# Kernel optimization log

Measured on AMD Instinct MI355X. Metric: run time of the kernel, lower is better.

The kernel has to match this reference:

```python
import jax, jax.numpy as jnp
import numpy as np

N_FLUID = 16384
N_BDY = 4096
E_F = 262144
E_B = 65536
F_IN = 4
B_IN = 4
RBF_N = 8
RBF_M = 8


def _tent_basis(x, n):
    # 'linear' RBF series: tent (hat) functions on n centers spanning [-1, 1]
    c = jnp.linspace(-1.0, 1.0, n, dtype=x.dtype)
    spacing = 2.0 / (n - 1)
    return jnp.maximum(0.0, 1.0 - jnp.abs(x[:, None] - c[None, :]) / spacing)  # [E, n]


def _polar_map(d):
    # coordinateMapping='polar': (dx,dy) -> (2*r-1, theta/pi), both ~[-1,1]
    r = jnp.sqrt(jnp.sum(d * d, axis=-1) + 1e-12)
    theta = jnp.arctan2(d[:, 1], d[:, 0])
    return jnp.stack([2.0 * r - 1.0, theta / np.pi], axis=-1)


def _rbf_conv(x_src, tgt_idx, src_idx, edge_dirs, W, num_targets):
    # Continuous RBF convolution: gather source feats along edges, weight by
    # separable RBF basis of the (mapped) edge direction, scatter-sum to targets.
    # W: [n, m, c_in, c_out]; edge_dirs: [E, 2]
    n, m, cin, cout = W.shape
    mapped = _polar_map(edge_dirs)
    bu = _tent_basis(mapped[:, 0], n)                     # [E, n]
    bv = _tent_basis(mapped[:, 1], m)                     # [E, m]
    b = (bu[:, :, None] * bv[:, None, :]).reshape(edge_dirs.shape[0], n * m)  # [E, K]
    xj = x_src[src_idx]                                   # [E, c_in]
    Wk = W.reshape(n * m, cin, cout)                      # [K, c_in, c_out]

    def step(acc, kv):
        bk, wk = kv                                       # [E], [c_in, c_out]
        return acc + bk[:, None] * (xj @ wk), None

    acc0 = jnp.zeros((xj.shape[0], cout), dtype=xj.dtype)
    msgs, _ = jax.lax.scan(step, acc0, (b.T, Wk))         # [E, c_out], no [E,K,c] blowup
    return jax.ops.segment_sum(msgs, tgt_idx, num_segments=num_targets)


def _forward(fp, bp, ff, bfeat, support, W0, W1, W2, W3, W4, fc0, fc1, fc2, fc3,
             fi, fj, bf, bb):
    nf = fp.shape[0]
    # edge direction features (post radius-search math of RbfNet.forward)
    flen = jnp.clip(-(fp[fj] - fp[fi]) / support, -1.0, 1.0)   # [E_F, 2]
    blen = jnp.clip((bp[bb] - fp[bf]) / support, -1.0, 1.0)    # [E_B, 2]

    lin = jax.nn.relu(ff @ fc0)                                      # [nf, 32]
    fconv = jax.nn.relu(_rbf_conv(ff, fi, fj, flen, W0, nf))         # [nf, 32]
    bconv = jax.nn.relu(_rbf_conv(bfeat, bf, bb, blen, W1, nf))      # [nf, 32]
    ans = jnp.concatenate([lin, fconv, bconv], axis=-1)              # [nf, 96]

    # layer i=2: features 32 != 64 -> no residual, relu
    ans = jax.nn.relu(_rbf_conv(ans, fi, fj, flen, W2, nf) + ans @ fc1)
    # layer i=3: 64 == 64 -> residual, relu
    ans = jax.nn.relu(_rbf_conv(ans, fi, fj, flen, W3, nf) + ans @ fc2 + ans)
    # layer i=4 (last): no residual (64 != 2), no relu
    ans = _rbf_conv(ans, fi, fj, flen, W4, nf) + ans @ fc3
    return ans                                                        # [nf, 2]


def setup_inputs() -> dict:
    key = jax.random.key(0)
    ks = jax.random.split(key, 20)

    def xavier(k, cin, cout):
        s = float(np.sqrt(2.0 / (cin + cout)))
        return jax.random.normal(k, (cin, cout), dtype=jnp.float32) * s

    def conv_w(k, n, m, cin, cout):
        s = float(np.sqrt(2.0 / (cin + cout)) / np.sqrt(n))
        return jax.random.normal(k, (n, m, cin, cout), dtype=jnp.float32) * s

    inp = {
        'fluidPositions': jax.random.uniform(ks[0], (N_FLUID, 2), dtype=jnp.float32),
        'boundaryPositions': jax.random.uniform(ks[1], (N_BDY, 2), dtype=jnp.float32),
        'fluidFeatures': jax.random.normal(ks[2], (N_FLUID, F_IN), dtype=jnp.float32),
        'boundaryFeatures': jax.random.normal(ks[3], (N_BDY, B_IN), dtype=jnp.float32),
        'support': jnp.asarray(1.5, dtype=jnp.float32),
        'fi': jax.random.randint(ks[4], (E_F,), 0, N_FLUID, dtype=jnp.int32),
        'fj': jax.random.randint(ks[5], (E_F,), 0, N_FLUID, dtype=jnp.int32),
        'bf': jax.random.randint(ks[6], (E_B,), 0, N_FLUID, dtype=jnp.int32),
        'bb': jax.random.randint(ks[7], (E_B,), 0, N_BDY, dtype=jnp.int32),
        'W0': conv_w(ks[8], RBF_N, RBF_M, F_IN, 32),
        'W1': conv_w(ks[9], RBF_N, RBF_M, B_IN, 32),
        'W2': conv_w(ks[10], RBF_N, RBF_M, 96, 64),
        'W3': conv_w(ks[11], RBF_N, RBF_M, 64, 64),
        'W4': conv_w(ks[12], RBF_N, RBF_M, 64, 2),
        'fc0': xavier(ks[13], F_IN, 32),
        'fc1': xavier(ks[14], 96, 64),
        'fc2': xavier(ks[15], 64, 64),
        'fc3': xavier(ks[16], 64, 2),
    }
    return inp


def reference(fluidPositions, boundaryPositions, fluidFeatures, boundaryFeatures,
              support, fi, fj, bf, bb, W0, W1, W2, W3, W4, fc0, fc1, fc2, fc3):
    return _forward(fluidPositions, boundaryPositions, fluidFeatures, boundaryFeatures,
                    support, W0, W1, W2, W3, W4, fc0, fc1, fc2, fc3, fi, fj, bf, bb)
```

## Files before the change

kernel.cpp:

```cpp
#include <hip/hip_runtime.h>

#define NF 16384
#define NB 4096
#define EF 262144
#define EB 65536
#define FBLK 1024
#define BBLK 256

typedef __attribute__((ext_vector_type(8))) short bf16x8;
typedef __attribute__((ext_vector_type(4))) float f32x4;

__device__ __forceinline__ short f2b(float f) {
  unsigned u = __float_as_uint(f);
  u += 0x7fff + ((u >> 16) & 1);
  return (short)(u >> 16);
}
__device__ __forceinline__ unsigned pack2(float lo, float hi) {
  return (unsigned)(unsigned short)f2b(lo) | ((unsigned)(unsigned short)f2b(hi) << 16);
}
__device__ __forceinline__ float b2f_lo(unsigned u) {
  return __uint_as_float(u << 16);
}
__device__ __forceinline__ float b2f_hi(unsigned u) {
  return __uint_as_float(u & 0xffff0000u);
}

__global__ void __launch_bounds__(256) dual_hist(const int* __restrict__ fi,
                                                 const int* __restrict__ bfi,
                                                 int* __restrict__ fhist,
                                                 int* __restrict__ bhist) {
  int bid = blockIdx.x;
  if (bid < FBLK) {
    int e = bid * 256 + threadIdx.x;
    atomicAdd(fhist + fi[e], 1);
  } else {
    int e = (bid - FBLK) * 256 + threadIdx.x;
    atomicAdd(bhist + bfi[e], 1);
  }
}

__global__ void __launch_bounds__(1024) csr_scan2(const int* __restrict__ fhist,
                                                  const int* __restrict__ bhist,
                                                  int* __restrict__ fstart, int* __restrict__ fcur,
                                                  int* __restrict__ bstart, int* __restrict__ bcur) {
  const int* hist = blockIdx.x ? bhist : fhist;
  int* start = blockIdx.x ? bstart : fstart;
  int* cursor = blockIdx.x ? bcur : fcur;
  __shared__ int wtot[16];
  int t = threadIdx.x;
  int lane = t & 63, wv = t >> 6;
  int base = t * 16;
  int vals[16];
  int s = 0;
#pragma unroll
  for (int k = 0; k < 16; k++) { vals[k] = hist[base + k]; s += vals[k]; }
  int ss = s;
  for (int off = 1; off < 64; off <<= 1) {
    int o = __shfl_up(ss, off, 64);
    if (lane >= off) ss += o;
  }
  if (lane == 63) wtot[wv] = ss;
  __syncthreads();
  if (t < 16) {
    int v = wtot[t];
    int vv = v;
    for (int off = 1; off < 16; off <<= 1) {
      int o = __shfl_up(vv, off, 64);
      if (t >= off) vv += o;
    }
    wtot[t] = vv - v;
  }
  __syncthreads();
  int run = ss - s + wtot[wv];
#pragma unroll
  for (int k = 0; k < 16; k++) { start[base + k] = run; cursor[base + k] = run; run += vals[k]; }
  if (t == 1023) start[16384] = run;
}

__global__ void __launch_bounds__(256) dual_scatter_payload(
    const int* __restrict__ fi, const int* __restrict__ fj,
    const int* __restrict__ bfi, const int* __restrict__ bb,
    const float* __restrict__ fp, const float* __restrict__ bp,
    const float* __restrict__ supportp,
    int* __restrict__ fcur, int* __restrict__ bcur,
    unsigned* __restrict__ fpk, float4* __restrict__ fwt,
    unsigned* __restrict__ bpk, float4* __restrict__ bwt) {
  int bid = blockIdx.x;
  bool fluid = bid < FBLK;
  int e = (fluid ? bid : bid - FBLK) * 256 + threadIdx.x;
  int ti = fluid ? fi[e] : bfi[e];
  int si = fluid ? fj[e] : bb[e];
  const float2* pT2 = (const float2*)fp;
  const float2* pS2 = fluid ? (const float2*)fp : (const float2*)bp;
  float sign = fluid ? -1.f : 1.f;
  float inv_sup = 1.0f / supportp[0];
  float2 pt = pT2[ti];
  float2 ps = pS2[si];
  float dx = sign * ((ps.x - pt.x) * inv_sup);
  float dy = sign * ((ps.y - pt.y) * inv_sup);
  dx = fminf(fmaxf(dx, -1.f), 1.f);
  dy = fminf(fmaxf(dy, -1.f), 1.f);
  float r = sqrtf(dx * dx + dy * dy + 1e-12f);
  float theta;
  if (dx == 0.0f && dy == 0.0f) {
    float mag = __builtin_signbitf(dx) ? 3.14159265358979323846f : 0.0f;
    theta = __builtin_signbitf(dy) ? -mag : mag;
  } else {
    theta = atan2f(dy, dx);
  }
  float u = 2.f * r - 1.f;
  float v = theta * (1.f / 3.14159265358979323846f);
  float tu = (u + 1.f) * 3.5f;
  float tv = (v + 1.f) * 3.5f;
  int iu = min(max((int)floorf(tu), 0), 6);
  int iv = min(max((int)floorf(tv), 0), 6);
  float wu0 = fmaxf(0.f, 1.f - fabsf(tu - (float)iu));
  float wu1 = fmaxf(0.f, 1.f - fabsf(tu - (float)(iu + 1)));
  float wv0 = fmaxf(0.f, 1.f - fabsf(tv - (float)iv));
  float wv1 = fmaxf(0.f, 1.f - fabsf(tv - (float)(iv + 1)));
  unsigned pk = (unsigned)si | ((unsigned)(iu * 8 + iv) << 14);
  float4 w4 = make_float4(wu0 * wv0, wu0 * wv1, wu1 * wv0, wu1 * wv1);
  if (fluid) {
    int p = atomicAdd(fcur + ti, 1);
    fpk[p] = pk; fwt[p] = w4;
  } else {
    int p = atomicAdd(bcur + ti, 1);
    bpk[p] = pk; bwt[p] = w4;
  }
}

__global__ void __launch_bounds__(256) build_weights(
    const float* __restrict__ W2, const float* __restrict__ W3,
    const float* __restrict__ W4, const float* __restrict__ W0,
    const float* __restrict__ W1,
    short* __restrict__ BT2, short* __restrict__ BT3, short* __restrict__ BT4,
    float* __restrict__ W0T, float* __restrict__ W1T) {
  int bid = blockIdx.x;
  if (bid < 1536) {
    int tid = bid * 256 + threadIdx.x;
    int k = tid % 96, n = tid / 96;
    BT2[tid] = f2b(W2[((size_t)(n >> 6) * 96 + k) * 64 + (n & 63)]);
  } else if (bid < 2560) {
    int tid = (bid - 1536) * 256 + threadIdx.x;
    int k = tid & 63, n = tid >> 6;
    BT3[tid] = f2b(W3[((size_t)(n >> 6) * 64 + k) * 64 + (n & 63)]);
  } else if (bid < 2592) {
    int tid = (bid - 2560) * 256 + threadIdx.x;
    int k = tid & 63, n = tid >> 6;
    BT4[tid] = f2b(W4[((size_t)(n >> 1) * 64 + k) * 2 + (n & 1)]);
  } else {
    int tid = (bid - 2592) * 256 + threadIdx.x;
    int cell = tid >> 7, r = tid & 127;
    int p = r >> 3, k = (r >> 1) & 3, c = r & 1;
    int dst = cell * 128 + p * 8 + k * 2 + c;
    int src = cell * 128 + k * 32 + 2 * p + c;
    W0T[dst] = W0[src];
    W1T[dst] = W1[src];
  }
}

template <int K>
__global__ void __launch_bounds__(256, 2) gemm_bf16(
    const short* __restrict__ A, const short* __restrict__ BT,
    short* __restrict__ C, int N) {
  constexpr int KP = K + 8;
  __shared__ __align__(16) short Al[128 * KP];
  __shared__ __align__(16) short Bl[128 * KP];
  int tid = threadIdx.x;
  int lane = tid & 63;
  int w = tid >> 6;
  int m0b = blockIdx.x * 128;
  int n0b = blockIdx.y * 128;
  constexpr int ROWV = K / 8;
  for (int f = tid; f < 128 * ROWV; f += 256) {
    int r = f / ROWV, c = f % ROWV;
    *(float4*)(Al + r * KP + c * 8) = *(const float4*)(A + (size_t)(m0b + r) * K + c * 8);
    *(float4*)(Bl + r * KP + c * 8) = *(const float4*)(BT + (size_t)(n0b + r) * K + c * 8);
  }
  __syncthreads();
  int m0 = (w & 1) * 64;
  int n0 = (w >> 1) * 64;
  int fr = lane & 15;
  int kg = lane >> 4;
  f32x4 acc[4][4] = {};
#pragma unroll
  for (int kc = 0; kc < K; kc += 32) {
    bf16x8 a[4], b[4];
#pragma unroll
    for (int i = 0; i < 4; i++) {
      a[i] = *(const bf16x8*)(Al + (m0 + i * 16 + fr) * KP + kc + kg * 8);
      b[i] = *(const bf16x8*)(Bl + (n0 + i * 16 + fr) * KP + kc + kg * 8);
    }
#pragma unroll
    for (int i = 0; i < 4; i++)
#pragma unroll
      for (int j = 0; j < 4; j++)
        acc[i][j] = __builtin_amdgcn_mfma_f32_16x16x32_bf16(a[i], b[j], acc[i][j], 0, 0, 0);
  }
#pragma unroll
  for (int i = 0; i < 4; i++) {
    int row = m0b + m0 + i * 16 + (lane >> 4) * 4;
#pragma unroll
    for (int j = 0; j < 4; j++) {
      int col = n0b + n0 + j * 16 + (lane & 15);
#pragma unroll
      for (int r = 0; r < 4; r++)
        C[(size_t)(row + r) * N + col] = f2b(acc[i][j][r]);
    }
  }
}

__global__ void __launch_bounds__(256, 8) b1_stage1(
    const float* __restrict__ ff, const float* __restrict__ bfe,
    const float* __restrict__ fc0,
    const float* __restrict__ W0T, const float* __restrict__ W1T,
    const int* __restrict__ ftstart, const unsigned* __restrict__ fpk,
    const float4* __restrict__ fwt,
    const int* __restrict__ btstart, const unsigned* __restrict__ bpk,
    const float4* __restrict__ bwt,
    float* __restrict__ ans0, short* __restrict__ Xh96) {
  int lane = threadIdx.x & 63;
  int t = __builtin_amdgcn_readfirstlane(blockIdx.x * 4 + (threadIdx.x >> 6));
  int q = lane >> 4;
  int p = lane & 15;
  int cofs = (q & 1) + (q >> 1) * 8;

  auto run_side = [&](const int* st, const unsigned* pkA, const float4* wtA,
                      const float* xA, const float* WT) -> float2 {
    float2 acc = make_float2(0.f, 0.f);
    int s = __builtin_amdgcn_readfirstlane(st[t]);
    int e1 = __builtin_amdgcn_readfirstlane(st[t + 1]);
    for (int base = s; base < e1; base += 64) {
      int Ln = min(64, e1 - base);
      unsigned mypk = 0;
      float4 myw = make_float4(0.f, 0.f, 0.f, 0.f);
      float4 myx = make_float4(0.f, 0.f, 0.f, 0.f);
      if (lane < Ln) {
        mypk = pkA[base + lane];
        myw = wtA[base + lane];
        myx = *(const float4*)(xA + (size_t)(mypk & 16383) * 4);
      }
      int j = 0;
      for (; j + 3 < Ln; j += 4) {
        unsigned pk_[4];
        float wq_[4], xx_[4], xy_[4], xz_[4], xw_[4];
#pragma unroll
        for (int u = 0; u < 4; u++) {
          pk_[u] = __shfl(mypk, j + u, 64);
          float wx = __shfl(myw.x, j + u, 64), wy = __shfl(myw.y, j + u, 64);
          float wz = __shfl(myw.z, j + u, 64), ww = __shfl(myw.w, j + u, 64);
          wq_[u] = (q == 0) ? wx : (q == 1) ? wy : (q == 2) ? wz : ww;
          xx_[u] = __shfl(myx.x, j + u, 64);
          xy_[u] = __shfl(myx.y, j + u, 64);
          xz_[u] = __shfl(myx.z, j + u, 64);
          xw_[u] = __shfl(myx.w, j + u, 64);
        }
        float4 A_[4], B_[4];
#pragma unroll
        for (int u = 0; u < 4; u++) {
          int cell = (int)(pk_[u] >> 14) + cofs;
          const float4* Wt = (const float4*)(WT + cell * 128 + p * 8);
          A_[u] = Wt[0];
          B_[u] = Wt[1];
        }
#pragma unroll
        for (int u = 0; u < 4; u++) {
          acc.x = fmaf(wq_[u],
                       xx_[u] * A_[u].x + xy_[u] * A_[u].z + xz_[u] * B_[u].x + xw_[u] * B_[u].z,
                       acc.x);
          acc.y = fmaf(wq_[u],
                       xx_[u] * A_[u].y + xy_[u] * A_[u].w + xz_[u] * B_[u].y + xw_[u] * B_[u].w,
                       acc.y);
        }
      }
      for (; j < Ln; j++) {
        unsigned pk = __shfl(mypk, j, 64);
        float wx = __shfl(myw.x, j, 64), wy = __shfl(myw.y, j, 64);
        float wz = __shfl(myw.z, j, 64), ww = __shfl(myw.w, j, 64);
        float xx = __shfl(myx.x, j, 64), xy = __shfl(myx.y, j, 64);
        float xz = __shfl(myx.z, j, 64), xw = __shfl(myx.w, j, 64);
        float wq = (q == 0) ? wx : (q == 1) ? wy : (q == 2) ? wz : ww;
        int cell = (int)(pk >> 14) + cofs;
        const float4* Wt = (const float4*)(WT + cell * 128 + p * 8);
        float4 A = Wt[0], B = Wt[1];
        acc.x = fmaf(wq, xx * A.x + xy * A.z + xz * B.x + xw * B.z, acc.x);
        acc.y = fmaf(wq, xx * A.y + xy * A.w + xz * B.y + xw * B.w, acc.y);
      }
    }
    return acc;
  };

  float2 fa = run_side(ftstart, fpk, fwt, ff, W0T);
  float2 ba = run_side(btstart, bpk, bwt, bfe, W1T);

  fa.x += __shfl_xor(fa.x, 16, 64); fa.y += __shfl_xor(fa.y, 16, 64);
  fa.x += __shfl_xor(fa.x, 32, 64); fa.y += __shfl_xor(fa.y, 32, 64);
  ba.x += __shfl_xor(ba.x, 16, 64); ba.y += __shfl_xor(ba.y, 16, 64);
  ba.x += __shfl_xor(ba.x, 32, 64); ba.y += __shfl_xor(ba.y, 32, 64);
  if (lane < 16) {
    fa.x = fmaxf(fa.x, 0.f); fa.y = fmaxf(fa.y, 0.f);
    *(float2*)(ans0 + (size_t)t * 96 + 32 + 2 * p) = fa;
    *(unsigned*)(Xh96 + (size_t)t * 96 + 32 + 2 * p) = pack2(fa.x, fa.y);
  } else if (lane < 32) {
    ba.x = fmaxf(ba.x, 0.f); ba.y = fmaxf(ba.y, 0.f);
    *(float2*)(ans0 + (size_t)t * 96 + 64 + 2 * p) = ba;
    *(unsigned*)(Xh96 + (size_t)t * 96 + 64 + 2 * p) = pack2(ba.x, ba.y);
  } else if (lane < 48) {
    float4 fv = *(const float4*)(ff + (size_t)t * 4);
    float l0 = fv.x * fc0[2 * p] + fv.y * fc0[32 + 2 * p] +
               fv.z * fc0[64 + 2 * p] + fv.w * fc0[96 + 2 * p];
    float l1 = fv.x * fc0[2 * p + 1] + fv.y * fc0[32 + 2 * p + 1] +
               fv.z * fc0[64 + 2 * p + 1] + fv.w * fc0[96 + 2 * p + 1];
    l0 = fmaxf(l0, 0.f); l1 = fmaxf(l1, 0.f);
    *(float2*)(ans0 + (size_t)t * 96 + 2 * p) = make_float2(l0, l1);
    *(unsigned*)(Xh96 + (size_t)t * 96 + 2 * p) = pack2(l0, l1);
  }
}

template <int CIN, int RESID, int WBF16>
__global__ void __launch_bounds__(256, 8) b23(
    const float* __restrict__ xin, const float* __restrict__ fc,
    const int* __restrict__ ftstart, const unsigned* __restrict__ epk,
    const float4* __restrict__ ewt, const short* __restrict__ Y,
    const float* __restrict__ resid, float* __restrict__ dest,
    short* __restrict__ Xh64, int c0, int CC, int init, int fin) {
  int lane = threadIdx.x & 63;
  int t = __builtin_amdgcn_readfirstlane(blockIdx.x * 4 + (threadIdx.x >> 6));
  int q = lane >> 4;
  int sub = lane & 15;
  int cofs = (q & 1) + (q >> 1) * 8;
  int YW = CC * 64;
  float a0 = 0.f, a1 = 0.f, a2 = 0.f, a3 = 0.f;
  if (init) {
    const float* xr = xin + (size_t)t * CIN;
#pragma unroll
    for (int kk = 0; kk < CIN / 4; kk++) {
      int k = q * (CIN / 4) + kk;
      float xv = xr[k];
      float4 fv = *(const float4*)(fc + (size_t)k * 64 + 4 * sub);
      a0 = fmaf(xv, fv.x, a0);
      a1 = fmaf(xv, fv.y, a1);
      a2 = fmaf(xv, fv.z, a2);
      a3 = fmaf(xv, fv.w, a3);
    }
  }
  int s = __builtin_amdgcn_readfirstlane(ftstart[t]);
  int e1 = __builtin_amdgcn_readfirstlane(ftstart[t + 1]);
  for (int base = s; base < e1; base += 64) {
    int Ln = min(64, e1 - base);
    unsigned mypk = 0;
    float4 myw = make_float4(0.f, 0.f, 0.f, 0.f);
    if (lane < Ln) {
      mypk = epk[base + lane];
      myw = ewt[base + lane];
    }
    int j = 0;
    for (; j + 7 < Ln; j += 8) {
      float wq_[8];
      uint2 r_[8];
#pragma unroll
      for (int u = 0; u < 8; u++) {
        unsigned pk = __shfl(mypk, j + u, 64);
        float wx = __shfl(myw.x, j + u, 64), wy = __shfl(myw.y, j + u, 64);
        float wz = __shfl(myw.z, j + u, 64), ww = __shfl(myw.w, j + u, 64);
        wq_[u] = (q == 0) ? wx : (q == 1) ? wy : (q == 2) ? wz : ww;
        int src = pk & 16383;
        int cell = (int)(pk >> 14) + cofs - c0;
        r_[u] = make_uint2(0, 0);
        if ((unsigned)cell < (unsigned)CC)
          r_[u] = *(const uint2*)(Y + (size_t)src * YW + cell * 64 + 4 * sub);
      }
#pragma unroll
      for (int u = 0; u < 8; u++) {
        a0 = fmaf(wq_[u], b2f_lo(r_[u].x), a0);
        a1 = fmaf(wq_[u], b2f_hi(r_[u].x), a1);
        a2 = fmaf(wq_[u], b2f_lo(r_[u].y), a2);
        a3 = fmaf(wq_[u], b2f_hi(r_[u].y), a3);
      }
    }
    for (; j < Ln; j++) {
      unsigned pk = __shfl(mypk, j, 64);
      float wx = __shfl(myw.x, j, 64), wy = __shfl(myw.y, j, 64);
      float wz = __shfl(myw.z, j, 64), ww = __shfl(myw.w, j, 64);
      float wq = (q == 0) ? wx : (q == 1) ? wy : (q == 2) ? wz : ww;
      int src = pk & 16383;
      int cell = (int)(pk >> 14) + cofs - c0;
      if ((unsigned)cell < (unsigned)CC) {
        uint2 r = *(const uint2*)(Y + (size_t)src * YW + cell * 64 + 4 * sub);
        a0 = fmaf(wq, b2f_lo(r.x), a0);
        a1 = fmaf(wq, b2f_hi(r.x), a1);
        a2 = fmaf(wq, b2f_lo(r.y), a2);
        a3 = fmaf(wq, b2f_hi(r.y), a3);
      }
    }
  }
  a0 += __shfl_xor(a0, 16, 64); a1 += __shfl_xor(a1, 16, 64);
  a2 += __shfl_xor(a2, 16, 64); a3 += __shfl_xor(a3, 16, 64);
  a0 += __shfl_xor(a0, 32, 64); a1 += __shfl_xor(a1, 32, 64);
  a2 += __shfl_xor(a2, 32, 64); a3 += __shfl_xor(a3, 32, 64);
  if (lane < 16) {
    float4* dst = (float4*)(dest + (size_t)t * 64 + 4 * sub);
    if (!init) {
      float4 d = *dst;
      a0 += d.x; a1 += d.y; a2 += d.z; a3 += d.w;
    }
    if (RESID && init) {
      float4 rd = *(const float4*)(resid + (size_t)t * 64 + 4 * sub);
      a0 += rd.x; a1 += rd.y; a2 += rd.z; a3 += rd.w;
    }
    if (fin) {
      a0 = fmaxf(a0, 0.f); a1 = fmaxf(a1, 0.f);
      a2 = fmaxf(a2, 0.f); a3 = fmaxf(a3, 0.f);
    }
    *dst = make_float4(a0, a1, a2, a3);
    if (WBF16 && fin) {
      uint2 pkd = make_uint2(pack2(a0, a1), pack2(a2, a3));
      *(uint2*)(Xh64 + (size_t)t * 64 + 4 * sub) = pkd;
    }
  }
}

__global__ void __launch_bounds__(256, 8) b4_stage4(
    const float* __restrict__ ans2, const float* __restrict__ fc3,
    const int* __restrict__ ftstart, const unsigned* __restrict__ epk,
    const float4* __restrict__ ewt, const short* __restrict__ Y4h,
    float* __restrict__ outp) {
  int lane = threadIdx.x & 63;
  int t = blockIdx.x * 4 + (threadIdx.x >> 6);
  int s4 = ftstart[t] * 4, e4 = ftstart[t + 1] * 4;
  float m0 = 0.f, m1 = 0.f;
  for (int fq = s4 + lane; fq < e4; fq += 64) {
    int idx = fq >> 2, j = fq & 3;
    unsigned pk = epk[idx];
    float4 w4 = ewt[idx];
    int src = pk & 16383;
    int cell = (int)(pk >> 14) + (j & 1) + (j >> 1) * 8;
    float w = (j == 0) ? w4.x : (j == 1) ? w4.y : (j == 2) ? w4.z : w4.w;
    unsigned mm = *(const unsigned*)(Y4h + (size_t)src * 128 + cell * 2);
    m0 = fmaf(w, b2f_lo(mm), m0);
    m1 = fmaf(w, b2f_hi(mm), m1);
  }
  {
    float a = ans2[(size_t)t * 64 + lane];
    m0 += a * fc3[lane * 2 + 0];
    m1 += a * fc3[lane * 2 + 1];
  }
#pragma unroll
  for (int off = 32; off > 0; off >>= 1) {
    m0 += __shfl_xor(m0, off, 64);
    m1 += __shfl_xor(m1, off, 64);
  }
  if (lane == 0) {
    outp[t * 2] = m0;
    outp[t * 2 + 1] = m1;
  }
}

extern "C" void kernel_launch(void* const* d_in, const int* in_sizes, int n_in,
                              void* d_out, int out_size, void* d_ws, size_t ws_size,
                              hipStream_t stream) {
  const float* fp  = (const float*)d_in[0];
  const float* bp  = (const float*)d_in[1];
  const float* ff  = (const float*)d_in[2];
  const float* bfe = (const float*)d_in[3];
  const float* sup = (const float*)d_in[4];
  const int* fi  = (const int*)d_in[5];
  const int* fj  = (const int*)d_in[6];
  const int* bfi = (const int*)d_in[7];
  const int* bb  = (const int*)d_in[8];
  const float* W0 = (const float*)d_in[9];
  const float* W1 = (const float*)d_in[10];
  const float* W2 = (const float*)d_in[11];
  const float* W3 = (const float*)d_in[12];
  const float* W4 = (const float*)d_in[13];
  const float* fc0 = (const float*)d_in[14];
  const float* fc1 = (const float*)d_in[15];
  const float* fc2 = (const float*)d_in[16];
  const float* fc3 = (const float*)d_in[17];
  float* out = (float*)d_out;

  char* w = (char*)d_ws;
  size_t off = 0;
  auto alloc = [&](size_t bytes) {
    char* p = w + off;
    off += (bytes + 255) & ~size_t(255);
    return p;
  };
  float* ans0   = (float*)alloc((size_t)NF * 96 * 4);
  float* ans1   = (float*)alloc((size_t)NF * 64 * 4);
  float* ans2   = (float*)alloc((size_t)NF * 64 * 4);
  int* fthist  = (int*)alloc((size_t)NF * 4);
  int* bthist  = (int*)alloc((size_t)NF * 4);
  int* ftstart = (int*)alloc((size_t)(NF + 1) * 4);
  int* ftcur   = (int*)alloc((size_t)NF * 4);
  int* btstart = (int*)alloc((size_t)(NF + 1) * 4);
  int* btcur   = (int*)alloc((size_t)NF * 4);
  unsigned* fpk  = (unsigned*)alloc((size_t)EF * 4);
  float4* fwtP   = (float4*)alloc((size_t)EF * 16);
  unsigned* bpk  = (unsigned*)alloc((size_t)EB * 4);
  float4* bwtP   = (float4*)alloc((size_t)EB * 16);
  short* Xh96  = (short*)alloc((size_t)NF * 96 * 2);
  short* Xh64  = (short*)alloc((size_t)NF * 64 * 2);
  short* Xh64b = (short*)alloc((size_t)NF * 64 * 2);
  short* BT2 = (short*)alloc((size_t)4096 * 96 * 2);
  short* BT3 = (short*)alloc((size_t)4096 * 64 * 2);
  short* BT4 = (short*)alloc((size_t)128 * 64 * 2);
  float* W0T = (float*)alloc((size_t)8192 * 4);
  float* W1T = (float*)alloc((size_t)8192 * 4);
  char* Yreg = w + off;
  size_t avail = (ws_size > off) ? (ws_size - off) : 0;
  size_t percell = (size_t)NF * 64 * 2;
  int CC = 64;
  while (CC > 8 && (size_t)CC * percell > avail) CC >>= 1;
  int S = 64 / CC;
  short* Y   = (short*)Yreg;
  short* Y4h = (short*)Yreg;

  hipMemsetAsync(fthist, 0, (size_t)NF * 8, stream);

  build_weights<<<2624, 256, 0, stream>>>(W2, W3, W4, W0, W1, BT2, BT3, BT4, W0T, W1T);
  dual_hist<<<FBLK + BBLK, 256, 0, stream>>>(fi, bfi, fthist, bthist);
  csr_scan2<<<2, 1024, 0, stream>>>(fthist, bthist, ftstart, ftcur, btstart, btcur);
  dual_scatter_payload<<<FBLK + BBLK, 256, 0, stream>>>(fi, fj, bfi, bb, fp, bp, sup,
                                                        ftcur, btcur, fpk, fwtP, bpk, bwtP);

  b1_stage1<<<NF / 4, 256, 0, stream>>>(ff, bfe, fc0, W0T, W1T,
                                        ftstart, fpk, fwtP, btstart, bpk, bwtP,
                                        ans0, Xh96);
  for (int c = 0; c < S; c++) {
    int c0 = c * CC;
    gemm_bf16<96><<<dim3(NF / 128, CC * 64 / 128), 256, 0, stream>>>(
        Xh96, BT2 + (size_t)c0 * 64 * 96, Y, CC * 64);
    b23<96, 0, 1><<<NF / 4, 256, 0, stream>>>(ans0, fc1, ftstart, fpk, fwtP,
                                              Y, nullptr, ans1, Xh64,
                                              c0, CC, c == 0, c == S - 1);
  }
  for (int c = 0; c < S; c++) {
    int c0 = c * CC;
    gemm_bf16<64><<<dim3(NF / 128, CC * 64 / 128), 256, 0, stream>>>(
        Xh64, BT3 + (size_t)c0 * 64 * 64, Y, CC * 64);
    b23<64, 1, 1><<<NF / 4, 256, 0, stream>>>(ans1, fc2, ftstart, fpk, fwtP,
                                              Y, ans1, ans2, Xh64b,
                                              c0, CC, c == 0, c == S - 1);
  }
  gemm_bf16<64><<<dim3(NF / 128, 1), 256, 0, stream>>>(Xh64b, BT4, Y4h, 128);
  b4_stage4<<<NF / 4, 256, 0, stream>>>(ans2, fc3, ftstart, fpk, fwtP, Y4h, out);
}
```

Baseline: 336.9 us.

## Bucket edge taps by target and cell-half so chunked passes skip unused taps

Each edge's four bilinear taps are expanded into separate (src|cell, weight) payload entries. These are sorted into a CSR keyed by target node and by which 32-cell half the tap falls in. The Y buffer is fixed at 32 cells, so the conv layers always run in two halves, and each half reads only its own taps instead of scanning every edge and masking out-of-range cells. This trades extra sort work (a histogram pass that also computes the basis, a larger scan, and payload that is four times bigger) for less redundant gathering and no per-tap shuffles in the aggregation kernels.

```diff
diff --git a/kernel.cpp b/kernel.cpp
--- a/kernel.cpp
+++ b/kernel.cpp
@@ -6,6 +6,8 @@
 #define EB 65536
 #define FBLK 1024
 #define BBLK 256
+#define CC 32
+#define YW (CC * 64)
 
 typedef __attribute__((ext_vector_type(8))) short bf16x8;
 typedef __attribute__((ext_vector_type(4))) float f32x4;
@@ -25,66 +27,14 @@
   return __uint_as_float(u & 0xffff0000u);
 }
 
-__global__ void __launch_bounds__(256) dual_hist(const int* __restrict__ fi,
-                                                 const int* __restrict__ bfi,
-                                                 int* __restrict__ fhist,
-                                                 int* __restrict__ bhist) {
-  int bid = blockIdx.x;
-  if (bid < FBLK) {
-    int e = bid * 256 + threadIdx.x;
-    atomicAdd(fhist + fi[e], 1);
-  } else {
-    int e = (bid - FBLK) * 256 + threadIdx.x;
-    atomicAdd(bhist + bfi[e], 1);
-  }
-}
-
-__global__ void __launch_bounds__(1024) csr_scan2(const int* __restrict__ fhist,
-                                                  const int* __restrict__ bhist,
-                                                  int* __restrict__ fstart, int* __restrict__ fcur,
-                                                  int* __restrict__ bstart, int* __restrict__ bcur) {
-  const int* hist = blockIdx.x ? bhist : fhist;
-  int* start = blockIdx.x ? bstart : fstart;
-  int* cursor = blockIdx.x ? bcur : fcur;
-  __shared__ int wtot[16];
-  int t = threadIdx.x;
-  int lane = t & 63, wv = t >> 6;
-  int base = t * 16;
-  int vals[16];
-  int s = 0;
-#pragma unroll
-  for (int k = 0; k < 16; k++) { vals[k] = hist[base + k]; s += vals[k]; }
-  int ss = s;
-  for (int off = 1; off < 64; off <<= 1) {
-    int o = __shfl_up(ss, off, 64);
-    if (lane >= off) ss += o;
-  }
-  if (lane == 63) wtot[wv] = ss;
-  __syncthreads();
-  if (t < 16) {
-    int v = wtot[t];
-    int vv = v;
-    for (int off = 1; off < 16; off <<= 1) {
-      int o = __shfl_up(vv, off, 64);
-      if (t >= off) vv += o;
-    }
-    wtot[t] = vv - v;
-  }
-  __syncthreads();
-  int run = ss - s + wtot[wv];
-#pragma unroll
-  for (int k = 0; k < 16; k++) { start[base + k] = run; cursor[base + k] = run; run += vals[k]; }
-  if (t == 1023) start[16384] = run;
-}
-
-__global__ void __launch_bounds__(256) dual_scatter_payload(
+__global__ void __launch_bounds__(256) basis_all(
     const int* __restrict__ fi, const int* __restrict__ fj,
     const int* __restrict__ bfi, const int* __restrict__ bb,
     const float* __restrict__ fp, const float* __restrict__ bp,
     const float* __restrict__ supportp,
-    int* __restrict__ fcur, int* __restrict__ bcur,
-    unsigned* __restrict__ fpk, float4* __restrict__ fwt,
-    unsigned* __restrict__ bpk, float4* __restrict__ bwt) {
+    unsigned char* __restrict__ fc00, float4* __restrict__ fw4,
+    unsigned char* __restrict__ bc00, float4* __restrict__ bw4,
+    int* __restrict__ fhist2, int* __restrict__ bhist2) {
   int bid = blockIdx.x;
   bool fluid = bid < FBLK;
   int e = (fluid ? bid : bid - FBLK) * 256 + threadIdx.x;
@@ -118,15 +68,91 @@
   float wu1 = fmaxf(0.f, 1.f - fabsf(tu - (float)(iu + 1)));
   float wv0 = fmaxf(0.f, 1.f - fabsf(tv - (float)iv));
   float wv1 = fmaxf(0.f, 1.f - fabsf(tv - (float)(iv + 1)));
-  unsigned pk = (unsigned)si | ((unsigned)(iu * 8 + iv) << 14);
+  int c00 = iu * 8 + iv;
   float4 w4 = make_float4(wu0 * wv0, wu0 * wv1, wu1 * wv0, wu1 * wv1);
+  int chLo = c00 >> 5;
+  int chHi = (c00 + 8) >> 5;
   if (fluid) {
-    int p = atomicAdd(fcur + ti, 1);
-    fpk[p] = pk; fwt[p] = w4;
+    fc00[e] = (unsigned char)c00; fw4[e] = w4;
+    if (chLo == chHi) {
+      atomicAdd(fhist2 + ti * 2 + chLo, 4);
+    } else {
+      atomicAdd(fhist2 + ti * 2 + chLo, 2);
+      atomicAdd(fhist2 + ti * 2 + chHi, 2);
+    }
   } else {
-    int p = atomicAdd(bcur + ti, 1);
-    bpk[p] = pk; bwt[p] = w4;
-  }
+    bc00[e] = (unsigned char)c00; bw4[e] = w4;
+    if (chLo == chHi) {
+      atomicAdd(bhist2 + ti * 2 + chLo, 4);
+    } else {
+      atomicAdd(bhist2 + ti * 2 + chLo, 2);
+      atomicAdd(bhist2 + ti * 2 + chHi, 2);
+    }
+  }
+}
+
+__global__ void __launch_bounds__(1024) csr_scan32(const int* __restrict__ fhist,
+                                                   const int* __restrict__ bhist,
+                                                   int* __restrict__ fstart, int* __restrict__ fcur,
+                                                   int* __restrict__ bstart, int* __restrict__ bcur) {
+  const int* hist = blockIdx.x ? bhist : fhist;
+  int* start = blockIdx.x ? bstart : fstart;
+  int* cursor = blockIdx.x ? bcur : fcur;
+  __shared__ int wtot[16];
+  int t = threadIdx.x;
+  int lane = t & 63, wv = t >> 6;
+  int base = t * 32;
+  int vals[32];
+  int s = 0;
+#pragma unroll
+  for (int k = 0; k < 32; k++) { vals[k] = hist[base + k]; s += vals[k]; }
+  int ss = s;
+  for (int off = 1; off < 64; off <<= 1) {
+    int o = __shfl_up(ss, off, 64);
+    if (lane >= off) ss += o;
+  }
+  if (lane == 63) wtot[wv] = ss;
+  __syncthreads();
+  if (t < 16) {
+    int v = wtot[t];
+    int vv = v;
+    for (int off = 1; off < 16; off <<= 1) {
+      int o = __shfl_up(vv, off, 64);
+      if (t >= off) vv += o;
+    }
+    wtot[t] = vv - v;
+  }
+  __syncthreads();
+  int run = ss - s + wtot[wv];
+#pragma unroll
+  for (int k = 0; k < 32; k++) { start[base + k] = run; cursor[base + k] = run; run += vals[k]; }
+  if (t == 1023) start[32768] = run;
+}
+
+__global__ void __launch_bounds__(256) scatter_pay(
+    const int* __restrict__ fi, const int* __restrict__ fj,
+    const int* __restrict__ bfi, const int* __restrict__ bb,
+    const unsigned char* __restrict__ fc00, const float4* __restrict__ fw4,
+    const unsigned char* __restrict__ bc00, const float4* __restrict__ bw4,
+    int* __restrict__ fcur2, int* __restrict__ bcur2,
+    uint2* __restrict__ fpay, uint2* __restrict__ bpay) {
+  int bid = blockIdx.x;
+  bool fluid = bid < FBLK;
+  int e = (fluid ? bid : bid - FBLK) * 256 + threadIdx.x;
+  int ti = fluid ? fi[e] : bfi[e];
+  unsigned src = (unsigned)(fluid ? fj[e] : bb[e]);
+  int c00 = (int)(fluid ? fc00[e] : bc00[e]);
+  float4 w4 = fluid ? fw4[e] : bw4[e];
+  int* cur2 = fluid ? fcur2 : bcur2;
+  uint2* pay = fluid ? fpay : bpay;
+  int chLo = c00 >> 5;
+  int chHi = (c00 + 8) >> 5;
+  int pLo = atomicAdd(cur2 + ti * 2 + chLo, 2);
+  pay[pLo]     = make_uint2(src | ((unsigned)c00 << 14), __float_as_uint(w4.x));
+  pay[pLo + 1] = make_uint2(src | ((unsigned)(c00 + 1) << 14), __float_as_uint(w4.y));
+  int pHi = atomicAdd(cur2 + ti * 2 + chHi, 2);
+  pay[pHi]     = make_uint2(src | ((unsigned)(c00 + 8) << 14), __float_as_uint(w4.z));
+  pay[pHi + 1] = make_uint2(src | ((unsigned)(c00 + 9) << 14), __float_as_uint(w4.w));
 }
 
 __global__ void __launch_bounds__(256) build_weights(
@@ -214,84 +240,53 @@
     const float* __restrict__ ff, const float* __restrict__ bfe,
     const float* __restrict__ fc0,
     const float* __restrict__ W0T, const float* __restrict__ W1T,
-    const int* __restrict__ ftstart, const unsigned* __restrict__ fpk,
-    const float4* __restrict__ fwt,
-    const int* __restrict__ btstart, const unsigned* __restrict__ bpk,
-    const float4* __restrict__ bwt,
+    const int* __restrict__ fstart2, const uint2* __restrict__ fpay,
+    const int* __restrict__ bstart2, const uint2* __restrict__ bpay,
     float* __restrict__ ans0, short* __restrict__ Xh96) {
   int lane = threadIdx.x & 63;
   int t = __builtin_amdgcn_readfirstlane(blockIdx.x * 4 + (threadIdx.x >> 6));
   int q = lane >> 4;
   int p = lane & 15;
-  int cofs = (q & 1) + (q >> 1) * 8;
-
-  auto run_side = [&](const int* st, const unsigned* pkA, const float4* wtA,
-                      const float* xA, const float* WT) -> float2 {
+
+  auto run_side = [&](int lo, int hi, const uint2* pay, const float* xA,
+                      const float* WT) -> float2 {
     float2 acc = make_float2(0.f, 0.f);
-    int s = __builtin_amdgcn_readfirstlane(st[t]);
-    int e1 = __builtin_amdgcn_readfirstlane(st[t + 1]);
-    for (int base = s; base < e1; base += 64) {
-      int Ln = min(64, e1 - base);
-      unsigned mypk = 0;
-      float4 myw = make_float4(0.f, 0.f, 0.f, 0.f);
-      float4 myx = make_float4(0.f, 0.f, 0.f, 0.f);
-      if (lane < Ln) {
-        mypk = pkA[base + lane];
-        myw = wtA[base + lane];
-        myx = *(const float4*)(xA + (size_t)(mypk & 16383) * 4);
+    for (int base = lo; base < hi; base += 16) {
+      float w_[4], xx_[4], xy_[4], xz_[4], xw_[4];
+      float4 A_[4], B_[4];
+#pragma unroll
+      for (int g = 0; g < 4; g++) {
+        int myi = base + g * 4 + q;
+        bool act = myi < hi;
+        uint2 pl = act ? pay[myi] : make_uint2(0u, 0u);
+        int src = pl.x & 16383;
+        int cell = (int)(pl.x >> 14);
+        w_[g] = __uint_as_float(pl.y);
+        float4 xv = *(const float4*)(xA + (size_t)src * 4);
+        xx_[g] = xv.x; xy_[g] = xv.y; xz_[g] = xv.z; xw_[g] = xv.w;
+        const float4* Wt = (const float4*)(WT + cell * 128 + p * 8);
+        A_[g] = Wt[0];
+        B_[g] = Wt[1];
       }
-      int j = 0;
-      for (; j + 3 < Ln; j += 4) {
-        unsigned pk_[4];
-        float wq_[4], xx_[4], xy_[4], xz_[4], xw_[4];
-#pragma unroll
-        for (int u = 0; u < 4; u++) {
-          pk_[u] = __shfl(mypk, j + u, 64);
-          float wx = __shfl(myw.x, j + u, 64), wy = __shfl(myw.y, j + u, 64);
-          float wz = __shfl(myw.z, j + u, 64), ww = __shfl(myw.w, j + u, 64);
-          wq_[u] = (q == 0) ? wx : (q == 1) ? wy : (q == 2) ? wz : ww;
-          xx_[u] = __shfl(myx.x, j + u, 64);
-          xy_[u] = __shfl(myx.y, j + u, 64);
-          xz_[u] = __shfl(myx.z, j + u, 64);
-          xw_[u] = __shfl(myx.w, j + u, 64);
-        }
-        float4 A_[4], B_[4];
-#pragma unroll
-        for (int u = 0; u < 4; u++) {
-          int cell = (int)(pk_[u] >> 14) + cofs;
-          const float4* Wt = (const float4*)(WT + cell * 128 + p * 8);
-          A_[u] = Wt[0];
-          B_[u] = Wt[1];
-        }
-#pragma unroll
-        for (int u = 0; u < 4; u++) {
-          acc.x = fmaf(wq_[u],
-                       xx_[u] * A_[u].x + xy_[u] * A_[u].z + xz_[u] * B_[u].x + xw_[u] * B_[u].z,
-                       acc.x);
-          acc.y = fmaf(wq_[u],
-                       xx_[u] * A_[u].y + xy_[u] * A_[u].w + xz_[u] * B_[u].y + xw_[u] * B_[u].w,
-                       acc.y);
-        }
-      }
-      for (; j < Ln; j++) {
-        unsigned pk = __shfl(mypk, j, 64);
-        float wx = __shfl(myw.x, j, 64), wy = __shfl(myw.y, j, 64);
-        float wz = __shfl(myw.z, j, 64), ww = __shfl(myw.w, j, 64);
-        float xx = __shfl(myx.x, j, 64), xy = __shfl(myx.y, j, 64);
-        float xz = __shfl(myx.z, j, 64), xw = __shfl(myx.w, j, 64);
-        float wq = (q == 0) ? wx : (q == 1) ? wy : (q == 2) ? wz : ww;
-        int cell = (int)(pk >> 14) + cofs;
-        const float4* Wt = (const float4*)(WT + cell * 128 + p * 8);
-        float4 A = Wt[0], B = Wt[1];
-        acc.x = fmaf(wq, xx * A.x + xy * A.z + xz * B.x + xw * B.z, acc.x);
-        acc.y = fmaf(wq, xx * A.y + xy * A.w + xz * B.y + xw * B.w, acc.y);
+#pragma unroll
+      for (int g = 0; g < 4; g++) {
+        acc.x = fmaf(w_[g],
+                     xx_[g] * A_[g].x + xy_[g] * A_[g].z + xz_[g] * B_[g].x + xw_[g] * B_[g].z,
+                     acc.x);
+        acc.y = fmaf(w_[g],
+                     xx_[g] * A_[g].y + xy_[g] * A_[g].w + xz_[g] * B_[g].y + xw_[g] * B_[g].w,
+                     acc.y);
       }
     }
     return acc;
   };
 
-  float2 fa = run_side(ftstart, fpk, fwt, ff, W0T);
-  float2 ba = run_side(btstart, bpk, bwt, bfe, W1T);
+  int flo = __builtin_amdgcn_readfirstlane(fstart2[2 * t]);
+  int fhi = __builtin_amdgcn_readfirstlane(fstart2[2 * t + 2]);
+  int blo = __builtin_amdgcn_readfirstlane(bstart2[2 * t]);
+  int bhi = __builtin_amdgcn_readfirstlane(bstart2[2 * t + 2]);
+  float2 fa = run_side(flo, fhi, fpay, ff, W0T);
+  float2 ba = run_side(blo, bhi, bpay, bfe, W1T);
 
   fa.x += __shfl_xor(fa.x, 16, 64); fa.y += __shfl_xor(fa.y, 16, 64);
   fa.x += __shfl_xor(fa.x, 32, 64); fa.y += __shfl_xor(fa.y, 32, 64);
@@ -318,18 +313,16 @@
 }
 
 template <int CIN, int RESID, int WBF16>
-__global__ void __launch_bounds__(256, 8) b23(
+__global__ void __launch_bounds__(256, 4) b23(
     const float* __restrict__ xin, const float* __restrict__ fc,
-    const int* __restrict__ ftstart, const unsigned* __restrict__ epk,
-    const float4* __restrict__ ewt, const short* __restrict__ Y,
-    const float* __restrict__ resid, float* __restrict__ dest,
-    short* __restrict__ Xh64, int c0, int CC, int init, int fin) {
+    const int* __restrict__ fstart2, const uint2* __restrict__ fpay,
+    const short* __restrict__ Y, const float* __restrict__ resid,
+    float* __restrict__ dest, short* __restrict__ Xh64,
+    int c0, int r, int init, int fin) {
   int lane = threadIdx.x & 63;
   int t = __builtin_amdgcn_readfirstlane(blockIdx.x * 4 + (threadIdx.x >> 6));
   int q = lane >> 4;
   int sub = lane & 15;
-  int cofs = (q & 1) + (q >> 1) * 8;
-  int YW = CC * 64;
   float a0 = 0.f, a1 = 0.f, a2 = 0.f, a3 = 0.f;
   if (init) {
     const float* xr = xin + (size_t)t * CIN;
@@ -344,54 +337,28 @@
       a3 = fmaf(xv, fv.w, a3);
     }
   }
-  int s = __builtin_amdgcn_readfirstlane(ftstart[t]);
-  int e1 = __builtin_amdgcn_readfirstlane(ftstart[t + 1]);
-  for (int base = s; base < e1; base += 64) {
-    int Ln = min(64, e1 - base);
-    unsigned mypk = 0;
-    float4 myw = make_float4(0.f, 0.f, 0.f, 0.f);
-    if (lane < Ln) {
-      mypk = epk[base + lane];
-      myw = ewt[base + lane];
-    }
-    int j = 0;
-    for (; j + 7 < Ln; j += 8) {
-      float wq_[8];
-      uint2 r_[8];
-#pragma unroll
-      for (int u = 0; u < 8; u++) {
-        unsigned pk = __shfl(mypk, j + u, 64);
-        float wx = __shfl(myw.x, j + u, 64), wy = __shfl(myw.y, j + u, 64);
-        float wz = __shfl(myw.z, j + u, 64), ww = __shfl(myw.w, j + u, 64);
-        wq_[u] = (q == 0) ? wx : (q == 1) ? wy : (q == 2) ? wz : ww;
-        int src = pk & 16383;
-        int cell = (int)(pk >> 14) + cofs - c0;
-        r_[u] = make_uint2(0, 0);
-        if ((unsigned)cell < (unsigned)CC)
-          r_[u] = *(const uint2*)(Y + (size_t)src * YW + cell * 64 + 4 * sub);
-      }
-#pragma unroll
-      for (int u = 0; u < 8; u++) {
-        a0 = fmaf(wq_[u], b2f_lo(r_[u].x), a0);
-        a1 = fmaf(wq_[u], b2f_hi(r_[u].x), a1);
-        a2 = fmaf(wq_[u], b2f_lo(r_[u].y), a2);
-        a3 = fmaf(wq_[u], b2f_hi(r_[u].y), a3);
-      }
-    }
-    for (; j < Ln; j++) {
-      unsigned pk = __shfl(mypk, j, 64);
-      float wx = __shfl(myw.x, j, 64), wy = __shfl(myw.y, j, 64);
-      float wz = __shfl(myw.z, j, 64), ww = __shfl(myw.w, j, 64);
-      float wq = (q == 0) ? wx : (q == 1) ? wy : (q == 2) ? wz : ww;
-      int src = pk & 16383;
-      int cell = (int)(pk >> 14) + cofs - c0;
-      if ((unsigned)cell < (unsigned)CC) {
-        uint2 r = *(const uint2*)(Y + (size_t)src * YW + cell * 64 + 4 * sub);
-        a0 = fmaf(wq, b2f_lo(r.x), a0);
-        a1 = fmaf(wq, b2f_hi(r.x), a1);
-        a2 = fmaf(wq, b2f_lo(r.y), a2);
-        a3 = fmaf(wq, b2f_hi(r.y), a3);
-      }
+  int lo = __builtin_amdgcn_readfirstlane(fstart2[2 * t + r]);
+  int hi = __builtin_amdgcn_readfirstlane(fstart2[2 * t + r + 1]);
+  for (int base = lo; base < hi; base += 32) {
+    float w_[8];
+    uint2 r_[8];
+#pragma unroll
+    for (int g = 0; g < 8; g++) {
+      int myi = base + g * 4 + q;
+      bool act = myi < hi;
+      uint2 pl = act ? fpay[myi] : make_uint2(0u, 0u);
+      int src = pl.x & 16383;
+      int cell = (int)(pl.x >> 14) - c0;
+      w_[g] = __uint_as_float(pl.y);
+      r_[g] = make_uint2(0u, 0u);
+      if (act) r_[g] = *(const uint2*)(Y + (size_t)src * YW + cell * 64 + 4 * sub);
+    }
+#pragma unroll
+    for (int g = 0; g < 8; g++) {
+      a0 = fmaf(w_[g], b2f_lo(r_[g].x), a0);
+      a1 = fmaf(w_[g], b2f_hi(r_[g].x), a1);
+      a2 = fmaf(w_[g], b2f_lo(r_[g].y), a2);
+      a3 = fmaf(w_[g], b2f_hi(r_[g].y), a3);
     }
   }
   a0 += __shfl_xor(a0, 16, 64); a1 += __shfl_xor(a1, 16, 64);
@@ -422,20 +389,17 @@
 
 __global__ void __launch_bounds__(256, 8) b4_stage4(
     const float* __restrict__ ans2, const float* __restrict__ fc3,
-    const int* __restrict__ ftstart, const unsigned* __restrict__ epk,
-    const float4* __restrict__ ewt, const short* __restrict__ Y4h,
-    float* __restrict__ outp) {
+    const int* __restrict__ fstart2, const uint2* __restrict__ fpay,
+    const short* __restrict__ Y4h, float* __restrict__ outp) {
   int lane = threadIdx.x & 63;
   int t = blockIdx.x * 4 + (threadIdx.x >> 6);
-  int s4 = ftstart[t] * 4, e4 = ftstart[t + 1] * 4;
+  int lo = fstart2[2 * t], hi = fstart2[2 * t + 2];
   float m0 = 0.f, m1 = 0.f;
-  for (int fq = s4 + lane; fq < e4; fq += 64) {
-    int idx = fq >> 2, j = fq & 3;
-    unsigned pk = epk[idx];
-    float4 w4 = ewt[idx];
-    int src = pk & 16383;
-    int cell = (int)(pk >> 14) + (j & 1) + (j >> 1) * 8;
-    float w = (j == 0) ? w4.x : (j == 1) ? w4.y : (j == 2) ? w4.z : w4.w;
+  for (int i = lo + lane; i < hi; i += 64) {
+    uint2 pl = fpay[i];
+    int src = pl.x & 16383;
+    int cell = (int)(pl.x >> 14);
+    float w = __uint_as_float(pl.y);
     unsigned mm = *(const unsigned*)(Y4h + (size_t)src * 128 + cell * 2);
     m0 = fmaf(w, b2f_lo(mm), m0);
     m1 = fmaf(w, b2f_hi(mm), m1);
@@ -489,16 +453,18 @@
   float* ans0   = (float*)alloc((size_t)NF * 96 * 4);
   float* ans1   = (float*)alloc((size_t)NF * 64 * 4);
   float* ans2   = (float*)alloc((size_t)NF * 64 * 4);
-  int* fthist  = (int*)alloc((size_t)NF * 4);
-  int* bthist  = (int*)alloc((size_t)NF * 4);
-  int* ftstart = (int*)alloc((size_t)(NF + 1) * 4);
-  int* ftcur   = (int*)alloc((size_t)NF * 4);
-  int* btstart = (int*)alloc((size_t)(NF + 1) * 4);
-  int* btcur   = (int*)alloc((size_t)NF * 4);
-  unsigned* fpk  = (unsigned*)alloc((size_t)EF * 4);
-  float4* fwtP   = (float4*)alloc((size_t)EF * 16);
-  unsigned* bpk  = (unsigned*)alloc((size_t)EB * 4);
-  float4* bwtP   = (float4*)alloc((size_t)EB * 16);
+  int* fhist2  = (int*)alloc((size_t)NF * 2 * 4);
+  int* bhist2  = (int*)alloc((size_t)NF * 2 * 4);
+  int* fstart2 = (int*)alloc((size_t)(NF * 2 + 1) * 4);
+  int* fcur2   = (int*)alloc((size_t)NF * 2 * 4);
+  int* bstart2 = (int*)alloc((size_t)(NF * 2 + 1) * 4);
+  int* bcur2   = (int*)alloc((size_t)NF * 2 * 4);
+  unsigned char* fc00 = (unsigned char*)alloc((size_t)EF);
+  float4* fw4  = (float4*)alloc((size_t)EF * 16);
+  unsigned char* bc00 = (unsigned char*)alloc((size_t)EB);
+  float4* bw4  = (float4*)alloc((size_t)EB * 16);
+  uint2* fpay  = (uint2*)alloc((size_t)EF * 4 * 8);
+  uint2* bpay  = (uint2*)alloc((size_t)EB * 4 * 8);
   short* Xh96  = (short*)alloc((size_t)NF * 96 * 2);
   short* Xh64  = (short*)alloc((size_t)NF * 64 * 2);
   short* Xh64b = (short*)alloc((size_t)NF * 64 * 2);
@@ -507,42 +473,36 @@
   short* BT4 = (short*)alloc((size_t)128 * 64 * 2);
   float* W0T = (float*)alloc((size_t)8192 * 4);
   float* W1T = (float*)alloc((size_t)8192 * 4);
-  char* Yreg = w + off;
-  size_t avail = (ws_size > off) ? (ws_size - off) : 0;
-  size_t percell = (size_t)NF * 64 * 2;
-  int CC = 64;
-  while (CC > 8 && (size_t)CC * percell > avail) CC >>= 1;
-  int S = 64 / CC;
-  short* Y   = (short*)Yreg;
-  short* Y4h = (short*)Yreg;
-
-  hipMemsetAsync(fthist, 0, (size_t)NF * 8, stream);
+  short* Y   = (short*)alloc((size_t)NF * YW * 2);
+  short* Y4h = Y;
+
+  hipMemsetAsync(fhist2, 0, (size_t)NF * 4 * 4, stream);
 
   build_weights<<<2624, 256, 0, stream>>>(W2, W3, W4, W0, W1, BT2, BT3, BT4, W0T, W1T);
-  dual_hist<<<FBLK + BBLK, 256, 0, stream>>>(fi, bfi, fthist, bthist);
-  csr_scan2<<<2, 1024, 0, stream>>>(fthist, bthist, ftstart, ftcur, btstart, btcur);
-  dual_scatter_payload<<<FBLK + BBLK, 256, 0, stream>>>(fi, fj, bfi, bb, fp, bp, sup,
-                                                        ftcur, btcur, fpk, fwtP, bpk, bwtP);
+  basis_all<<<FBLK + BBLK, 256, 0, stream>>>(fi, fj, bfi, bb, fp, bp, sup,
+                                             fc00, fw4, bc00, bw4, fhist2, bhist2);
+  csr_scan32<<<2, 1024, 0, stream>>>(fhist2, bhist2, fstart2, fcur2, bstart2, bcur2);
+  scatter_pay<<<FBLK + BBLK, 256, 0, stream>>>(fi, fj, bfi, bb, fc00, fw4, bc00, bw4,
+                                               fcur2, bcur2, fpay, bpay);
 
   b1_stage1<<<NF / 4, 256, 0, stream>>>(ff, bfe, fc0, W0T, W1T,
-                                        ftstart, fpk, fwtP, btstart, bpk, bwtP,
-                                        ans0, Xh96);
-  for (int c = 0; c < S; c++) {
-    int c0 = c * CC;
-    gemm_bf16<96><<<dim3(NF / 128, CC * 64 / 128), 256, 0, stream>>>(
-        Xh96, BT2 + (size_t)c0 * 64 * 96, Y, CC * 64);
-    b23<96, 0, 1><<<NF / 4, 256, 0, stream>>>(ans0, fc1, ftstart, fpk, fwtP,
+                                        fstart2, fpay, bstart2, bpay, ans0, Xh96);
+  for (int r = 0; r < 2; r++) {
+    int c0 = r * CC;
+    gemm_bf16<96><<<dim3(NF / 128, YW / 128), 256, 0, stream>>>(
+        Xh96, BT2 + (size_t)c0 * 64 * 96, Y, YW);
+    b23<96, 0, 1><<<NF / 4, 256, 0, stream>>>(ans0, fc1, fstart2, fpay,
                                               Y, nullptr, ans1, Xh64,
-                                              c0, CC, c == 0, c == S - 1);
-  }
-  for (int c = 0; c < S; c++) {
-    int c0 = c * CC;
-    gemm_bf16<64><<<dim3(NF / 128, CC * 64 / 128), 256, 0, stream>>>(
-        Xh64, BT3 + (size_t)c0 * 64 * 64, Y, CC * 64);
-    b23<64, 1, 1><<<NF / 4, 256, 0, stream>>>(ans1, fc2, ftstart, fpk, fwtP,
+                                              c0, r, r == 0, r == 1);
+  }
+  for (int r = 0; r < 2; r++) {
+    int c0 = r * CC;
+    gemm_bf16<64><<<dim3(NF / 128, YW / 128), 256, 0, stream>>>(
+        Xh64, BT3 + (size_t)c0 * 64 * 64, Y, YW);
+    b23<64, 1, 1><<<NF / 4, 256, 0, stream>>>(ans1, fc2, fstart2, fpay,
                                               Y, ans1, ans2, Xh64b,
-                                              c0, CC, c == 0, c == S - 1);
+                                              c0, r, r == 0, r == 1);
   }
   gemm_bf16<64><<<dim3(NF / 128, 1), 256, 0, stream>>>(Xh64b, BT4, Y4h, 128);
-  b4_stage4<<<NF / 4, 256, 0, stream>>>(ans2, fc3, ftstart, fpk, fwtP, Y4h, out);
-}
+  b4_stage4<<<NF / 4, 256, 0, stream>>>(ans2, fc3, fstart2, fpay, Y4h, out);
+}
```

Measured after the change: 396.4 us. 1.18x slower.
